# Kernel tuning notes

Measured on AMD Instinct MI355X. Metric: run time of the kernel, lower is better.

Reference implementation:

```python
import jax, jax.numpy as jnp
import numpy as np

HEADS = 8

def setup_inputs() -> dict:
    key = jax.random.key(0)
    k1, k2, k3 = jax.random.split(key, 3)
    B, C, L = 8, 512, 4096
    dim_head = 64
    hidden = HEADS * dim_head  # 512
    x = jax.random.normal(k1, (B, C, L), dtype=jnp.float32)
    # Conv1d(dim, hidden*3, 1, bias=False) -> weight [hidden*3, dim]
    w_qkv = jax.random.normal(k2, (hidden * 3, C), dtype=jnp.float32) * 0.02
    # Conv1d(hidden, dim, 1) -> weight [dim, hidden], bias [dim]
    w_out = jax.random.normal(k3, (C, hidden), dtype=jnp.float32) * 0.02
    b_out = jnp.zeros((C,), dtype=jnp.float32)
    return {"x": x, "w_qkv": w_qkv, "w_out": w_out, "b_out": b_out}

def reference(x, w_qkv, w_out, b_out):
    B, C, L = x.shape
    # 1x1 Conv1d == channel matmul
    qkv = jnp.einsum('oc,bcl->bol', w_qkv, x)            # [B, 3*H*dh, L]
    qkv = qkv.reshape(B, 3, HEADS, -1, L)                # qkv outermost, then heads, then c
    q, k, v = qkv[:, 0], qkv[:, 1], qkv[:, 2]            # each [B, H, dh, L]
    k = jax.nn.softmax(k, axis=-1)                       # softmax over sequence
    context = jnp.einsum('bhdn,bhen->bhde', k, v)        # [B, H, dh, dh]
    out = jnp.einsum('bhde,bhdn->bhen', context, q)      # [B, H, dh, L]
    out = out.reshape(B, -1, L)                          # [B, H*dh, L]
    return jnp.einsum('oc,bcl->bol', w_out, out) + b_out[None, :, None]
```

## Files before the change

### kernel.cpp

```cpp
#include <hip/hip_runtime.h>
#include <hip/hip_bf16.h>


typedef __bf16 bf16x8 __attribute__((ext_vector_type(8)));
typedef __bf16 bf16x4 __attribute__((ext_vector_type(4)));
typedef float  f32x4  __attribute__((ext_vector_type(4)));

#define B_  8
#define L_  4096
#define C_  512

#define GLD_LDS16(g, l)                                             \
    __builtin_amdgcn_global_load_lds(                               \
        (const __attribute__((address_space(1))) void*)(g),         \
        (__attribute__((address_space(3))) void*)(l), 16, 0, 0)

#define FENCE asm volatile("" ::: "memory")
#define BAR   do { FENCE; __builtin_amdgcn_s_barrier(); FENCE; } while (0)
#define DRAIN_LGKM asm volatile("s_waitcnt lgkmcnt(0)" ::: "memory")
#define WAIT_VM(N) asm volatile("s_waitcnt vmcnt(" #N ")" ::: "memory")

__global__ __launch_bounds__(256) void prep_all(const float* __restrict__ x,
                                                __hip_bfloat16* __restrict__ xt,
                                                const float* __restrict__ wqkv_f,
                                                __hip_bfloat16* __restrict__ wkv_b,
                                                __hip_bfloat16* __restrict__ wqT) {
    __shared__ float tile[64 * 132];
    int blk = blockIdx.x;
    int t = threadIdx.x;
    if (blk < 2048) {
        int b = blk >> 8, rem = blk & 255;
        int l0 = (rem & 31) * 128, c0 = (rem >> 5) * 64;
        const float* xp = x + ((size_t)b * C_ + c0) * L_ + l0;
#pragma unroll
        for (int p = 0; p < 8; p++) {
            int i = p * 8 + (t >> 5);
            int j = (t & 31) * 4;
            float4 vv = *(const float4*)(xp + (size_t)i * L_ + j);
            *(float4*)&tile[i * 132 + j] = vv;
        }
        __syncthreads();
        unsigned short* xo = (unsigned short*)xt + ((size_t)b * L_ + l0) * C_ + c0;
#pragma unroll
        for (int qq = 0; qq < 8; qq++) {
            int l = qq * 16 + (t >> 4);
            int cg = (t & 15) * 4;
            bf16x4 ov;
#pragma unroll
            for (int k = 0; k < 4; k++) ov[k] = (__bf16)tile[(cg + k) * 132 + l];
            *(bf16x4*)(xo + (size_t)l * C_ + cg) = ov;
        }
    } else if (blk < 4096) {
        int i = (blk - 2048) * 256 + t;
        wkv_b[i] = __float2bfloat16(wqkv_f[512 * 512 + i]);
    } else {
        int tb = blk - 4096;
        int r0 = (tb >> 4) * 32, c0 = (tb & 15) * 32;
        int tx = t & 31, ty = t >> 5;
        for (int r = 0; r < 32; r += 8)
            tile[(ty + r) * 33 + tx] = wqkv_f[(size_t)(r0 + ty + r) * 512 + c0 + tx];
        __syncthreads();
        for (int r = 0; r < 32; r += 8)
            wqT[(size_t)(c0 + ty + r) * 512 + r0 + tx] = __float2bfloat16(tile[tx * 33 + ty + r]);
    }
}

__global__ __launch_bounds__(256, 2) void gemm_kv(
    const __hip_bfloat16* __restrict__ A, const __hip_bfloat16* __restrict__ Bt,
    float* __restrict__ ctxp, float* __restrict__ Sp) {
    __shared__ alignas(16) unsigned short sA[2][128 * 64];
    __shared__ alignas(16) unsigned short sB[2][128 * 64];
    __shared__ float Sred[64];

    const int K = C_;
    int b = blockIdx.z, h = blockIdx.y, slice = blockIdx.x;
    const __hip_bfloat16* Bb = Bt + (size_t)b * L_ * C_;

    int t = threadIdx.x;
    int lane = t & 63, wv = t >> 6;
    int l16 = lane & 15, q4 = lane >> 4;
    int wr = (wv >> 1) * 64, wc = (wv & 1) * 64;

    int srow = lane >> 3;
    int swz  = ((lane & 7) ^ srow) * 8;

    if (t < 64) Sred[t] = 0.f;

    const __hip_bfloat16* gA[4];
    unsigned ldoff[4];
    int rloc[4];
#pragma unroll
    for (int c = 0; c < 4; c++) {
        int r = c * 32 + wv * 8;
        int lr = r + srow;
        int grow = h * 64 + lr + (lr >= 64 ? 448 : 0);
        gA[c] = A + (size_t)grow * K + swz;
        ldoff[c] = (unsigned)r * 64;
        rloc[c] = lr;
    }

    int gsel0 = (q4 ^ (l16 & 7)) * 8;
    int gsel1 = gsel0 ^ 32;
    unsigned rA = (unsigned)(wr + l16) * 64;
    unsigned rB = (unsigned)(wc + l16) * 64;
    const int NKT = K >> 6;

    f32x4 acc2[4] = {};
    bf16x8 aF[4][2], bF[4][2];

#pragma unroll 1
    for (int sub = 0; sub < 4; ++sub) {
        int nt = slice * 512 + sub * 128;
        const __hip_bfloat16* gB[4];
#pragma unroll
        for (int c = 0; c < 4; c++)
            gB[c] = Bb + (size_t)(nt + rloc[c]) * K + swz;

        f32x4 acc[4][4] = {};

#pragma unroll
        for (int c = 0; c < 4; c++) GLD_LDS16(gA[c], &sA[0][ldoff[c]]);
#pragma unroll
        for (int c = 0; c < 4; c++) GLD_LDS16(gB[c], &sB[0][ldoff[c]]);
#pragma unroll
        for (int c = 0; c < 4; c++) GLD_LDS16(gA[c] + 64, &sA[1][ldoff[c]]);
        WAIT_VM(4);
        BAR;

#pragma unroll 1
        for (int kt = 0; kt < NKT; ++kt) {
            int cur = kt & 1, nbuf = cur ^ 1;
            const unsigned short* As_b = sA[cur];
            const unsigned short* Bs_b = sB[cur];
            bool st1 = (kt + 1) < NKT;
            bool st2 = (kt + 2) < NKT;

#pragma unroll
            for (int i = 0; i < 4; i++) {
                aF[i][0] = *(const bf16x8*)&As_b[rA + i * 1024 + gsel0];
                aF[i][1] = *(const bf16x8*)&As_b[rA + i * 1024 + gsel1];
            }
#pragma unroll
            for (int j = 0; j < 2; j++) {
                bF[j][0] = *(const bf16x8*)&Bs_b[rB + j * 1024 + gsel0];
                bF[j][1] = *(const bf16x8*)&Bs_b[rB + j * 1024 + gsel1];
            }
            if (st1) {
                int ko = (kt + 1) << 6;
#pragma unroll
                for (int c = 0; c < 4; c++) GLD_LDS16(gB[c] + ko, &sB[nbuf][ldoff[c]]);
            }
            BAR;
            __builtin_amdgcn_s_setprio(1);
#pragma unroll
            for (int ks = 0; ks < 2; ks++)
#pragma unroll
                for (int i = 0; i < 4; i++)
#pragma unroll
                    for (int j = 0; j < 2; j++)
                        acc[i][j] = __builtin_amdgcn_mfma_f32_16x16x32_bf16(aF[i][ks], bF[j][ks], acc[i][j], 0, 0, 0);
            __builtin_amdgcn_s_setprio(0);
            DRAIN_LGKM;
            BAR;

#pragma unroll
            for (int j = 2; j < 4; j++) {
                bF[j][0] = *(const bf16x8*)&Bs_b[rB + j * 1024 + gsel0];
                bF[j][1] = *(const bf16x8*)&Bs_b[rB + j * 1024 + gsel1];
            }
            if (st2) {
                int ko = (kt + 2) << 6;
#pragma unroll
                for (int c = 0; c < 4; c++) GLD_LDS16(gA[c] + ko, &sA[cur][ldoff[c]]);
            }
            BAR;
            __builtin_amdgcn_s_setprio(1);
#pragma unroll
            for (int ks = 0; ks < 2; ks++)
#pragma unroll
                for (int i = 0; i < 4; i++)
#pragma unroll
                    for (int j = 0; j < 2; j++)
                        acc[i][2 + j] = __builtin_amdgcn_mfma_f32_16x16x32_bf16(aF[i][ks], bF[2 + j][ks], acc[i][2 + j], 0, 0, 0);
            __builtin_amdgcn_s_setprio(0);
            DRAIN_LGKM;
            if (st2) { WAIT_VM(4); } else { WAIT_VM(0); }
            BAR;
        }

        __bf16* Pb = (__bf16*)sA;
        __bf16* Vb = (__bf16*)sB;

        if (wv < 2) {
#pragma unroll
            for (int i = 0; i < 4; i++)
#pragma unroll
                for (int r = 0; r < 4; r++) {
                    int d = i * 16 + q4 * 4 + r;
                    float rs = 0.f;
#pragma unroll
                    for (int j = 0; j < 4; j++) {
                        int n = wc + j * 16 + l16;
                        float pv = __expf(acc[i][j][r]);
                        rs += pv;
                        Pb[d * 128 + (((n >> 3) ^ (d & 15)) * 8) + (n & 7)] = (__bf16)pv;
                    }
                    rs += __shfl_xor(rs, 1, 64);
                    rs += __shfl_xor(rs, 2, 64);
                    rs += __shfl_xor(rs, 4, 64);
                    rs += __shfl_xor(rs, 8, 64);
                    if (l16 == 0) atomicAdd(&Sred[d], rs);
                }
        } else {
#pragma unroll
            for (int i = 0; i < 4; i++)
#pragma unroll
                for (int j = 0; j < 4; j++)
#pragma unroll
                    for (int r = 0; r < 4; r++) {
                        int e = i * 16 + q4 * 4 + r;
                        int n = wc + j * 16 + l16;
                        Vb[e * 128 + (((n >> 3) ^ (e & 15)) * 8) + (n & 7)] = (__bf16)acc[i][j][r];
                    }
        }
        DRAIN_LGKM;
        BAR;

#pragma unroll
        for (int kk = 0; kk < 4; kk++) {
            int gg = kk * 4 + q4;
            bf16x8 bf2 = *(const bf16x8*)&Vb[(wv * 16 + l16) * 128 + ((gg ^ l16) * 8)];
#pragma unroll
            for (int i2 = 0; i2 < 4; i2++) {
                bf16x8 af2 = *(const bf16x8*)&Pb[(i2 * 16 + l16) * 128 + ((gg ^ l16) * 8)];
                acc2[i2] = __builtin_amdgcn_mfma_f32_16x16x32_bf16(af2, bf2, acc2[i2], 0, 0, 0);
            }
        }
        DRAIN_LGKM;
        BAR;
    }

    float* cg = ctxp + ((size_t)slice * 64 + b * 8 + h) * 4096;
#pragma unroll
    for (int i2 = 0; i2 < 4; i2++)
#pragma unroll
        for (int r = 0; r < 4; r++) {
            int d = i2 * 16 + q4 * 4 + r;
            int e = wv * 16 + l16;
            cg[d * 64 + e] = acc2[i2][r];
        }
    if (t < 64)
        Sp[((size_t)slice * 64 + b * 8 + h) * 64 + t] = Sred[t];
}

__global__ __launch_bounds__(256, 2) void gemm_p(
    const __hip_bfloat16* __restrict__ A, const __hip_bfloat16* __restrict__ Bt,
    size_t strideA, size_t strideB, int M, int N, int K,
    float* __restrict__ outb, const float* __restrict__ bias) {
    __shared__ alignas(16) unsigned short sA[2][128 * 64];
    __shared__ alignas(16) unsigned short sB[2][128 * 64];

    int b = blockIdx.z;
    int m0 = blockIdx.y * 128, n0 = blockIdx.x * 128;
    const __hip_bfloat16* Ab = A + strideA * (size_t)b;
    const __hip_bfloat16* Bb = Bt + strideB * (size_t)b;

    int t = threadIdx.x;
    int lane = t & 63, wv = t >> 6;
    int l16 = lane & 15, q4 = lane >> 4;
    int wr = (wv >> 1) * 64, wc = (wv & 1) * 64;

    int srow = lane >> 3;
    int swz  = ((lane & 7) ^ srow) * 8;

    const __hip_bfloat16* gA[4];
    const __hip_bfloat16* gB[4];
    unsigned ldoff[4];
#pragma unroll
    for (int c = 0; c < 4; c++) {
        int r = c * 32 + wv * 8;
        gA[c] = Ab + (size_t)(m0 + r + srow) * K + swz;
        gB[c] = Bb + (size_t)(n0 + r + srow) * K + swz;
        ldoff[c] = (unsigned)r * 64;
    }

    int gsel0 = (q4 ^ (l16 & 7)) * 8;
    int gsel1 = gsel0 ^ 32;
    unsigned rA = (unsigned)(wr + l16) * 64;
    unsigned rB = (unsigned)(wc + l16) * 64;
    int NKT = K >> 6;

    f32x4 acc[4][4] = {};
    bf16x8 aF[4][2], bF[4][2];

#pragma unroll
    for (int c = 0; c < 4; c++) GLD_LDS16(gA[c], &sA[0][ldoff[c]]);
#pragma unroll
    for (int c = 0; c < 4; c++) GLD_LDS16(gB[c], &sB[0][ldoff[c]]);
    if (NKT > 1) {
#pragma unroll
        for (int c = 0; c < 4; c++) GLD_LDS16(gA[c] + 64, &sA[1][ldoff[c]]);
        WAIT_VM(4);
    } else {
        WAIT_VM(0);
    }
    BAR;

#pragma unroll 1
    for (int kt = 0; kt < NKT; ++kt) {
        int cur = kt & 1, nbuf = cur ^ 1;
        const unsigned short* As_b = sA[cur];
        const unsigned short* Bs_b = sB[cur];
        bool st1 = (kt + 1) < NKT;
        bool st2 = (kt + 2) < NKT;

#pragma unroll
        for (int i = 0; i < 4; i++) {
            aF[i][0] = *(const bf16x8*)&As_b[rA + i * 1024 + gsel0];
            aF[i][1] = *(const bf16x8*)&As_b[rA + i * 1024 + gsel1];
        }
#pragma unroll
        for (int j = 0; j < 2; j++) {
            bF[j][0] = *(const bf16x8*)&Bs_b[rB + j * 1024 + gsel0];
            bF[j][1] = *(const bf16x8*)&Bs_b[rB + j * 1024 + gsel1];
        }
        if (st1) {
            int ko = (kt + 1) << 6;
#pragma unroll
            for (int c = 0; c < 4; c++) GLD_LDS16(gB[c] + ko, &sB[nbuf][ldoff[c]]);
        }
        BAR;
        __builtin_amdgcn_s_setprio(1);
#pragma unroll
        for (int ks = 0; ks < 2; ks++)
#pragma unroll
            for (int i = 0; i < 4; i++)
#pragma unroll
                for (int j = 0; j < 2; j++)
                    acc[i][j] = __builtin_amdgcn_mfma_f32_16x16x32_bf16(aF[i][ks], bF[j][ks], acc[i][j], 0, 0, 0);
        __builtin_amdgcn_s_setprio(0);
        DRAIN_LGKM;
        BAR;

#pragma unroll
        for (int j = 2; j < 4; j++) {
            bF[j][0] = *(const bf16x8*)&Bs_b[rB + j * 1024 + gsel0];
            bF[j][1] = *(const bf16x8*)&Bs_b[rB + j * 1024 + gsel1];
        }
        if (st2) {
            int ko = (kt + 2) << 6;
#pragma unroll
            for (int c = 0; c < 4; c++) GLD_LDS16(gA[c] + ko, &sA[cur][ldoff[c]]);
        }
        BAR;
        __builtin_amdgcn_s_setprio(1);
#pragma unroll
        for (int ks = 0; ks < 2; ks++)
#pragma unroll
            for (int i = 0; i < 4; i++)
#pragma unroll
                for (int j = 0; j < 2; j++)
                    acc[i][2 + j] = __builtin_amdgcn_mfma_f32_16x16x32_bf16(aF[i][ks], bF[2 + j][ks], acc[i][2 + j], 0, 0, 0);
        __builtin_amdgcn_s_setprio(0);
        DRAIN_LGKM;
        if (st2) { WAIT_VM(4); } else { WAIT_VM(0); }
        BAR;
    }

#pragma unroll
    for (int i = 0; i < 4; i++)
#pragma unroll
        for (int j = 0; j < 4; j++)
#pragma unroll
            for (int r = 0; r < 4; r++) {
                int row = m0 + wr + i * 16 + q4 * 4 + r;
                int col = n0 + wc + j * 16 + l16;
                outb[((size_t)b * M + row) * (size_t)N + col] = acc[i][j][r] + bias[row];
            }
}

__global__ __launch_bounds__(256) void gemm_bt(
    const __hip_bfloat16* __restrict__ A, const __hip_bfloat16* __restrict__ Bt,
    size_t strideA, size_t strideB, int M, int N, int K,
    __hip_bfloat16* __restrict__ obf) {
    __shared__ alignas(16) unsigned short As[128 * 64];
    __shared__ alignas(16) unsigned short Bs[128 * 64];

    int b = blockIdx.z;
    int m0 = blockIdx.y * 128, n0 = blockIdx.x * 128;
    const __hip_bfloat16* Ab = A + strideA * (size_t)b;
    const __hip_bfloat16* Bb = Bt + strideB * (size_t)b;

    int t = threadIdx.x;
    int lane = t & 63, wv = t >> 6;
    int l16 = lane & 15, q4 = lane >> 4;
    int wr = (wv >> 1) * 64, wc = (wv & 1) * 64;

    int srow = lane >> 3;
    int swz  = ((lane & 7) ^ srow) * 8;

    const __hip_bfloat16* gA[4];
    const __hip_bfloat16* gB[4];
    unsigned short* lA[4];
    unsigned short* lB[4];
#pragma unroll
    for (int c = 0; c < 4; c++) {
        int r = wv * 32 + c * 8;
        gA[c] = Ab + (size_t)(m0 + r + srow) * K + swz;
        gB[c] = Bb + (size_t)(n0 + r + srow) * K + swz;
        lA[c] = &As[r * 64];
        lB[c] = &Bs[r * 64];
    }

    int gsel0 = ((q4) ^ (l16 & 7)) * 8;
    int gsel1 = gsel0 ^ 32;
    int rA = (wr + l16) * 64;
    int rB = (wc + l16) * 64;

    f32x4 acc[4][4] = {};

    for (int k0 = 0; k0 < K; k0 += 64) {
        __syncthreads();
#pragma unroll
        for (int c = 0; c < 4; c++) {
            GLD_LDS16(gA[c] + k0, lA[c]);
            GLD_LDS16(gB[c] + k0, lB[c]);
        }
        __syncthreads();

        bf16x8 af[4], bfr[4];
#pragma unroll
        for (int i = 0; i < 4; i++) {
            af[i]  = *(const bf16x8*)&As[rA + i * 1024 + gsel0];
            bfr[i] = *(const bf16x8*)&Bs[rB + i * 1024 + gsel0];
        }
#pragma unroll
        for (int i = 0; i < 4; i++)
#pragma unroll
            for (int j = 0; j < 4; j++)
                acc[i][j] = __builtin_amdgcn_mfma_f32_16x16x32_bf16(af[i], bfr[j], acc[i][j], 0, 0, 0);
#pragma unroll
        for (int i = 0; i < 4; i++) {
            af[i]  = *(const bf16x8*)&As[rA + i * 1024 + gsel1];
            bfr[i] = *(const bf16x8*)&Bs[rB + i * 1024 + gsel1];
        }
#pragma unroll
        for (int i = 0; i < 4; i++)
#pragma unroll
            for (int j = 0; j < 4; j++)
                acc[i][j] = __builtin_amdgcn_mfma_f32_16x16x32_bf16(af[i], bfr[j], acc[i][j], 0, 0, 0);
    }

#pragma unroll
    for (int i = 0; i < 4; i++)
#pragma unroll
        for (int j = 0; j < 4; j++)
#pragma unroll
            for (int r = 0; r < 4; r++) {
                int row = m0 + wr + i * 16 + q4 * 4 + r;
                int col = n0 + wc + j * 16 + l16;
                obf[((size_t)b * 512 + row) * (size_t)N + col] = __float2bfloat16(acc[i][j][r]);
            }
}

__global__ __launch_bounds__(256) void w2_kernel(const float* __restrict__ wout,
                                                 const float* __restrict__ ctxp,
                                                 const float* __restrict__ Sp,
                                                 __hip_bfloat16* __restrict__ w2) {
    int ob = blockIdx.x, h = blockIdx.y, b = blockIdx.z;
    __shared__ float cT[64 * 65];
    __shared__ float wT[64 * 65];
    __shared__ float Sinv[64];
    int t = threadIdx.x;
    const size_t SL = (size_t)64 * 4096;
    const float* cg = ctxp + ((size_t)b * 8 + h) * 4096;
    if (t < 64) {
        const float* sg = Sp + ((size_t)b * 8 + h) * 64;
        float S = 0.f;
#pragma unroll
        for (int s = 0; s < 8; s++) S += sg[(size_t)s * 64 * 64 + t];
        Sinv[t] = 1.0f / S;
    }
    __syncthreads();
    for (int i = t; i < 4096; i += 256) {
        int d = i >> 6, e = i & 63;
        float s = 0.f;
#pragma unroll
        for (int sl = 0; sl < 8; sl++) s += cg[(size_t)sl * SL + i];
        cT[e * 65 + d] = s * Sinv[d];
        wT[e * 65 + d] = wout[(size_t)(ob * 64 + d) * 512 + h * 64 + e];
    }
    __syncthreads();
    int ol = t >> 2;
    int db = (t & 3) * 16;
    unsigned short* w2p = (unsigned short*)w2 + ((size_t)b * 512 + ob * 64 + ol) * 512 + h * 64;
    for (int g = 0; g < 4; g++) {
        int d0 = db + g * 4;
        float s0 = 0.f, s1 = 0.f, s2 = 0.f, s3 = 0.f;
#pragma unroll
        for (int e = 0; e < 64; e++) {
            float w = wT[e * 65 + ol];
            s0 += w * cT[e * 65 + d0];
            s1 += w * cT[e * 65 + d0 + 1];
            s2 += w * cT[e * 65 + d0 + 2];
            s3 += w * cT[e * 65 + d0 + 3];
        }
        bf16x4 ov;
        ov[0] = (__bf16)s0; ov[1] = (__bf16)s1; ov[2] = (__bf16)s2; ov[3] = (__bf16)s3;
        *(bf16x4*)(w2p + d0) = ov;
    }
}

extern "C" void kernel_launch(void* const* d_in, const int* in_sizes, int n_in,
                              void* d_out, int out_size, void* d_ws, size_t ws_size,
                              hipStream_t stream) {
    const float* x     = (const float*)d_in[0];
    const float* w_qkv = (const float*)d_in[1];
    const float* w_out = (const float*)d_in[2];
    const float* b_out = (const float*)d_in[3];
    float* out = (float*)d_out;
    char* ws = (char*)d_ws;

    size_t off_xt   = 0;
    size_t off_wkv  = off_xt + (size_t)B_ * L_ * C_ * 2;
    size_t off_wqT  = off_wkv + (size_t)1024 * 512 * 2;
    size_t off_ctxp = off_wqT + (size_t)512 * 512 * 2;
    size_t off_Sp   = off_ctxp + (size_t)8 * 64 * 4096 * 4;
    size_t off_w2   = off_Sp + (size_t)8 * 64 * 64 * 4;
    size_t off_w3   = off_w2 + (size_t)B_ * 512 * 512 * 2;

    __hip_bfloat16* xt   = (__hip_bfloat16*)(ws + off_xt);
    __hip_bfloat16* wkvb = (__hip_bfloat16*)(ws + off_wkv);
    __hip_bfloat16* wqT  = (__hip_bfloat16*)(ws + off_wqT);
    float*          ctxp = (float*)(ws + off_ctxp);
    float*          Sp   = (float*)(ws + off_Sp);
    __hip_bfloat16* w2   = (__hip_bfloat16*)(ws + off_w2);
    __hip_bfloat16* W3   = (__hip_bfloat16*)(ws + off_w3);

    prep_all<<<4352, 256, 0, stream>>>(x, xt, w_qkv, wkvb, wqT);

    gemm_kv<<<dim3(8, 8, B_), 256, 0, stream>>>(wkvb, xt, ctxp, Sp);

    w2_kernel<<<dim3(8, 8, B_), 256, 0, stream>>>(w_out, ctxp, Sp, w2);

    gemm_bt<<<dim3(512 / 128, 512 / 128, B_), 256, 0, stream>>>(
        w2, wqT, (size_t)512 * 512, 0, 512, 512, 512, W3);

    gemm_p<<<dim3(L_ / 128, 512 / 128, B_), 256, 0, stream>>>(
        W3, xt, (size_t)512 * 512, (size_t)L_ * C_, 512, L_, 512, out, b_out);
}
```

Baseline: 287.7 us.

## Split KV context GEMM across more blocks and add separate context reduction kernel

The kv GEMM is re-gridded from 8 slices, each looping over four 128-column sub-tiles, to 32 independent blocks per (batch, head), one 128-column tile each. This raises parallelism from 512 to 2048 blocks. A new ctxred kernel sums the 32 partial contexts, and w2_kernel now reads the reduced context with vectorised loads. The W2×Wq GEMM reuses the double-buffered gemm_p template in place of the simpler gemm_bt, and the x transpose writes 8-wide bf16 stores with a padded LDS stride. The cost is more partial-sum traffic and one extra launch.

```diff
diff --git a/kernel.cpp b/kernel.cpp
--- a/kernel.cpp
+++ b/kernel.cpp
@@ -25,7 +25,7 @@
                                                 const float* __restrict__ wqkv_f,
                                                 __hip_bfloat16* __restrict__ wkv_b,
                                                 __hip_bfloat16* __restrict__ wqT) {
-    __shared__ float tile[64 * 132];
+    __shared__ float tile[64 * 133];
     int blk = blockIdx.x;
     int t = threadIdx.x;
     if (blk < 2048) {
@@ -37,18 +37,18 @@
             int i = p * 8 + (t >> 5);
             int j = (t & 31) * 4;
             float4 vv = *(const float4*)(xp + (size_t)i * L_ + j);
-            *(float4*)&tile[i * 132 + j] = vv;
+            *(float4*)&tile[i * 133 + j] = vv;
         }
         __syncthreads();
         unsigned short* xo = (unsigned short*)xt + ((size_t)b * L_ + l0) * C_ + c0;
-#pragma unroll
-        for (int qq = 0; qq < 8; qq++) {
-            int l = qq * 16 + (t >> 4);
-            int cg = (t & 15) * 4;
-            bf16x4 ov;
-#pragma unroll
-            for (int k = 0; k < 4; k++) ov[k] = (__bf16)tile[(cg + k) * 132 + l];
-            *(bf16x4*)(xo + (size_t)l * C_ + cg) = ov;
+        int cg8 = (t & 7) * 8;
+#pragma unroll
+        for (int qq = 0; qq < 4; qq++) {
+            int l = qq * 32 + (t >> 3);
+            bf16x8 ov;
+#pragma unroll
+            for (int k = 0; k < 8; k++) ov[k] = (__bf16)tile[(cg8 + k) * 133 + l];
+            *(bf16x8*)(xo + (size_t)l * C_ + cg8) = ov;
         }
     } else if (blk < 4096) {
         int i = (blk - 2048) * 256 + t;
@@ -73,7 +73,8 @@
     __shared__ float Sred[64];
 
     const int K = C_;
-    int b = blockIdx.z, h = blockIdx.y, slice = blockIdx.x;
+    int b = blockIdx.z, h = blockIdx.y, nt = blockIdx.x;
+    int n0 = nt * 128;
     const __hip_bfloat16* Bb = Bt + (size_t)b * L_ * C_;
 
     int t = threadIdx.x;
@@ -87,16 +88,16 @@
     if (t < 64) Sred[t] = 0.f;
 
     const __hip_bfloat16* gA[4];
+    const __hip_bfloat16* gB[4];
     unsigned ldoff[4];
-    int rloc[4];
 #pragma unroll
     for (int c = 0; c < 4; c++) {
         int r = c * 32 + wv * 8;
         int lr = r + srow;
         int grow = h * 64 + lr + (lr >= 64 ? 448 : 0);
         gA[c] = A + (size_t)grow * K + swz;
+        gB[c] = Bb + (size_t)(n0 + lr) * K + swz;
         ldoff[c] = (unsigned)r * 64;
-        rloc[c] = lr;
     }
 
     int gsel0 = (q4 ^ (l16 & 7)) * 8;
@@ -105,191 +106,6 @@
     unsigned rB = (unsigned)(wc + l16) * 64;
     const int NKT = K >> 6;
 
-    f32x4 acc2[4] = {};
-    bf16x8 aF[4][2], bF[4][2];
-
-#pragma unroll 1
-    for (int sub = 0; sub < 4; ++sub) {
-        int nt = slice * 512 + sub * 128;
-        const __hip_bfloat16* gB[4];
-#pragma unroll
-        for (int c = 0; c < 4; c++)
-            gB[c] = Bb + (size_t)(nt + rloc[c]) * K + swz;
-
-        f32x4 acc[4][4] = {};
-
-#pragma unroll
-        for (int c = 0; c < 4; c++) GLD_LDS16(gA[c], &sA[0][ldoff[c]]);
-#pragma unroll
-        for (int c = 0; c < 4; c++) GLD_LDS16(gB[c], &sB[0][ldoff[c]]);
-#pragma unroll
-        for (int c = 0; c < 4; c++) GLD_LDS16(gA[c] + 64, &sA[1][ldoff[c]]);
-        WAIT_VM(4);
-        BAR;
-
-#pragma unroll 1
-        for (int kt = 0; kt < NKT; ++kt) {
-            int cur = kt & 1, nbuf = cur ^ 1;
-            const unsigned short* As_b = sA[cur];
-            const unsigned short* Bs_b = sB[cur];
-            bool st1 = (kt + 1) < NKT;
-            bool st2 = (kt + 2) < NKT;
-
-#pragma unroll
-            for (int i = 0; i < 4; i++) {
-                aF[i][0] = *(const bf16x8*)&As_b[rA + i * 1024 + gsel0];
-                aF[i][1] = *(const bf16x8*)&As_b[rA + i * 1024 + gsel1];
-            }
-#pragma unroll
-            for (int j = 0; j < 2; j++) {
-                bF[j][0] = *(const bf16x8*)&Bs_b[rB + j * 1024 + gsel0];
-                bF[j][1] = *(const bf16x8*)&Bs_b[rB + j * 1024 + gsel1];
-            }
-            if (st1) {
-                int ko = (kt + 1) << 6;
-#pragma unroll
-                for (int c = 0; c < 4; c++) GLD_LDS16(gB[c] + ko, &sB[nbuf][ldoff[c]]);
-            }
-            BAR;
-            __builtin_amdgcn_s_setprio(1);
-#pragma unroll
-            for (int ks = 0; ks < 2; ks++)
-#pragma unroll
-                for (int i = 0; i < 4; i++)
-#pragma unroll
-                    for (int j = 0; j < 2; j++)
-                        acc[i][j] = __builtin_amdgcn_mfma_f32_16x16x32_bf16(aF[i][ks], bF[j][ks], acc[i][j], 0, 0, 0);
-            __builtin_amdgcn_s_setprio(0);
-            DRAIN_LGKM;
-            BAR;
-
-#pragma unroll
-            for (int j = 2; j < 4; j++) {
-                bF[j][0] = *(const bf16x8*)&Bs_b[rB + j * 1024 + gsel0];
-                bF[j][1] = *(const bf16x8*)&Bs_b[rB + j * 1024 + gsel1];
-            }
-            if (st2) {
-                int ko = (kt + 2) << 6;
-#pragma unroll
-                for (int c = 0; c < 4; c++) GLD_LDS16(gA[c] + ko, &sA[cur][ldoff[c]]);
-            }
-            BAR;
-            __builtin_amdgcn_s_setprio(1);
-#pragma unroll
-            for (int ks = 0; ks < 2; ks++)
-#pragma unroll
-                for (int i = 0; i < 4; i++)
-#pragma unroll
-                    for (int j = 0; j < 2; j++)
-                        acc[i][2 + j] = __builtin_amdgcn_mfma_f32_16x16x32_bf16(aF[i][ks], bF[2 + j][ks], acc[i][2 + j], 0, 0, 0);
-            __builtin_amdgcn_s_setprio(0);
-            DRAIN_LGKM;
-            if (st2) { WAIT_VM(4); } else { WAIT_VM(0); }
-            BAR;
-        }
-
-        __bf16* Pb = (__bf16*)sA;
-        __bf16* Vb = (__bf16*)sB;
-
-        if (wv < 2) {
-#pragma unroll
-            for (int i = 0; i < 4; i++)
-#pragma unroll
-                for (int r = 0; r < 4; r++) {
-                    int d = i * 16 + q4 * 4 + r;
-                    float rs = 0.f;
-#pragma unroll
-                    for (int j = 0; j < 4; j++) {
-                        int n = wc + j * 16 + l16;
-                        float pv = __expf(acc[i][j][r]);
-                        rs += pv;
-                        Pb[d * 128 + (((n >> 3) ^ (d & 15)) * 8) + (n & 7)] = (__bf16)pv;
-                    }
-                    rs += __shfl_xor(rs, 1, 64);
-                    rs += __shfl_xor(rs, 2, 64);
-                    rs += __shfl_xor(rs, 4, 64);
-                    rs += __shfl_xor(rs, 8, 64);
-                    if (l16 == 0) atomicAdd(&Sred[d], rs);
-                }
-        } else {
-#pragma unroll
-            for (int i = 0; i < 4; i++)
-#pragma unroll
-                for (int j = 0; j < 4; j++)
-#pragma unroll
-                    for (int r = 0; r < 4; r++) {
-                        int e = i * 16 + q4 * 4 + r;
-                        int n = wc + j * 16 + l16;
-                        Vb[e * 128 + (((n >> 3) ^ (e & 15)) * 8) + (n & 7)] = (__bf16)acc[i][j][r];
-                    }
-        }
-        DRAIN_LGKM;
-        BAR;
-
-#pragma unroll
-        for (int kk = 0; kk < 4; kk++) {
-            int gg = kk * 4 + q4;
-            bf16x8 bf2 = *(const bf16x8*)&Vb[(wv * 16 + l16) * 128 + ((gg ^ l16) * 8)];
-#pragma unroll
-            for (int i2 = 0; i2 < 4; i2++) {
-                bf16x8 af2 = *(const bf16x8*)&Pb[(i2 * 16 + l16) * 128 + ((gg ^ l16) * 8)];
-                acc2[i2] = __builtin_amdgcn_mfma_f32_16x16x32_bf16(af2, bf2, acc2[i2], 0, 0, 0);
-            }
-        }
-        DRAIN_LGKM;
-        BAR;
-    }
-
-    float* cg = ctxp + ((size_t)slice * 64 + b * 8 + h) * 4096;
-#pragma unroll
-    for (int i2 = 0; i2 < 4; i2++)
-#pragma unroll
-        for (int r = 0; r < 4; r++) {
-            int d = i2 * 16 + q4 * 4 + r;
-            int e = wv * 16 + l16;
-            cg[d * 64 + e] = acc2[i2][r];
-        }
-    if (t < 64)
-        Sp[((size_t)slice * 64 + b * 8 + h) * 64 + t] = Sred[t];
-}
-
-__global__ __launch_bounds__(256, 2) void gemm_p(
-    const __hip_bfloat16* __restrict__ A, const __hip_bfloat16* __restrict__ Bt,
-    size_t strideA, size_t strideB, int M, int N, int K,
-    float* __restrict__ outb, const float* __restrict__ bias) {
-    __shared__ alignas(16) unsigned short sA[2][128 * 64];
-    __shared__ alignas(16) unsigned short sB[2][128 * 64];
-
-    int b = blockIdx.z;
-    int m0 = blockIdx.y * 128, n0 = blockIdx.x * 128;
-    const __hip_bfloat16* Ab = A + strideA * (size_t)b;
-    const __hip_bfloat16* Bb = Bt + strideB * (size_t)b;
-
-    int t = threadIdx.x;
-    int lane = t & 63, wv = t >> 6;
-    int l16 = lane & 15, q4 = lane >> 4;
-    int wr = (wv >> 1) * 64, wc = (wv & 1) * 64;
-
-    int srow = lane >> 3;
-    int swz  = ((lane & 7) ^ srow) * 8;
-
-    const __hip_bfloat16* gA[4];
-    const __hip_bfloat16* gB[4];
-    unsigned ldoff[4];
-#pragma unroll
-    for (int c = 0; c < 4; c++) {
-        int r = c * 32 + wv * 8;
-        gA[c] = Ab + (size_t)(m0 + r + srow) * K + swz;
-        gB[c] = Bb + (size_t)(n0 + r + srow) * K + swz;
-        ldoff[c] = (unsigned)r * 64;
-    }
-
-    int gsel0 = (q4 ^ (l16 & 7)) * 8;
-    int gsel1 = gsel0 ^ 32;
-    unsigned rA = (unsigned)(wr + l16) * 64;
-    unsigned rB = (unsigned)(wc + l16) * 64;
-    int NKT = K >> 6;
-
     f32x4 acc[4][4] = {};
     bf16x8 aF[4][2], bF[4][2];
 
@@ -297,13 +113,9 @@
     for (int c = 0; c < 4; c++) GLD_LDS16(gA[c], &sA[0][ldoff[c]]);
 #pragma unroll
     for (int c = 0; c < 4; c++) GLD_LDS16(gB[c], &sB[0][ldoff[c]]);
-    if (NKT > 1) {
-#pragma unroll
-        for (int c = 0; c < 4; c++) GLD_LDS16(gA[c] + 64, &sA[1][ldoff[c]]);
-        WAIT_VM(4);
-    } else {
-        WAIT_VM(0);
-    }
+#pragma unroll
+    for (int c = 0; c < 4; c++) GLD_LDS16(gA[c] + 64, &sA[1][ldoff[c]]);
+    WAIT_VM(4);
     BAR;
 
 #pragma unroll 1
@@ -367,24 +179,93 @@
         BAR;
     }
 
-#pragma unroll
-    for (int i = 0; i < 4; i++)
-#pragma unroll
-        for (int j = 0; j < 4; j++)
+    __bf16* Pb = (__bf16*)sA;
+    __bf16* Vb = (__bf16*)sB;
+
+    if (wv < 2) {
+#pragma unroll
+        for (int i = 0; i < 4; i++)
 #pragma unroll
             for (int r = 0; r < 4; r++) {
-                int row = m0 + wr + i * 16 + q4 * 4 + r;
-                int col = n0 + wc + j * 16 + l16;
-                outb[((size_t)b * M + row) * (size_t)N + col] = acc[i][j][r] + bias[row];
+                int d = i * 16 + q4 * 4 + r;
+                float rs = 0.f;
+#pragma unroll
+                for (int j = 0; j < 4; j++) {
+                    int n = wc + j * 16 + l16;
+                    float pv = __expf(acc[i][j][r]);
+                    rs += pv;
+                    Pb[d * 128 + (((n >> 3) ^ (d & 15)) * 8) + (n & 7)] = (__bf16)pv;
+                }
+                rs += __shfl_xor(rs, 1, 64);
+                rs += __shfl_xor(rs, 2, 64);
+                rs += __shfl_xor(rs, 4, 64);
+                rs += __shfl_xor(rs, 8, 64);
+                if (l16 == 0) atomicAdd(&Sred[d], rs);
             }
-}
-
-__global__ __launch_bounds__(256) void gemm_bt(
+    } else {
+#pragma unroll
+        for (int i = 0; i < 4; i++)
+#pragma unroll
+            for (int j = 0; j < 4; j++)
+#pragma unroll
+                for (int r = 0; r < 4; r++) {
+                    int e = i * 16 + q4 * 4 + r;
+                    int n = wc + j * 16 + l16;
+                    Vb[e * 128 + (((n >> 3) ^ (e & 15)) * 8) + (n & 7)] = (__bf16)acc[i][j][r];
+                }
+    }
+    DRAIN_LGKM;
+    BAR;
+
+    f32x4 acc2[4] = {};
+#pragma unroll
+    for (int kk = 0; kk < 4; kk++) {
+        int gg = kk * 4 + q4;
+        bf16x8 bf2 = *(const bf16x8*)&Vb[(wv * 16 + l16) * 128 + ((gg ^ l16) * 8)];
+#pragma unroll
+        for (int i2 = 0; i2 < 4; i2++) {
+            bf16x8 af2 = *(const bf16x8*)&Pb[(i2 * 16 + l16) * 128 + ((gg ^ l16) * 8)];
+            acc2[i2] = __builtin_amdgcn_mfma_f32_16x16x32_bf16(af2, bf2, acc2[i2], 0, 0, 0);
+        }
+    }
+
+    float* cg = ctxp + ((size_t)nt * 64 + b * 8 + h) * 4096;
+#pragma unroll
+    for (int i2 = 0; i2 < 4; i2++)
+#pragma unroll
+        for (int r = 0; r < 4; r++) {
+            int d = i2 * 16 + q4 * 4 + r;
+            int e = wv * 16 + l16;
+            cg[d * 64 + e] = acc2[i2][r];
+        }
+    if (t < 64)
+        Sp[((size_t)nt * 64 + b * 8 + h) * 64 + t] = Sred[t];
+}
+
+__global__ __launch_bounds__(256) void ctxred(const float* __restrict__ ctxp,
+                                              float* __restrict__ ctxs) {
+    int q = blockIdx.x;
+    int bh = blockIdx.y;
+    int t = threadIdx.x;
+    int i0 = q * 1024 + t * 4;
+    const float* cg = ctxp + (size_t)bh * 4096 + i0;
+    float4 s = {0.f, 0.f, 0.f, 0.f};
+#pragma unroll
+    for (int sl = 0; sl < 32; sl++) {
+        float4 v = *(const float4*)(cg + (size_t)sl * 64 * 4096);
+        s.x += v.x; s.y += v.y; s.z += v.z; s.w += v.w;
+    }
+    *(float4*)(ctxs + (size_t)bh * 4096 + i0) = s;
+}
+
+template <int MODE>
+__global__ __launch_bounds__(256, 2) void gemm_p(
     const __hip_bfloat16* __restrict__ A, const __hip_bfloat16* __restrict__ Bt,
     size_t strideA, size_t strideB, int M, int N, int K,
-    __hip_bfloat16* __restrict__ obf) {
-    __shared__ alignas(16) unsigned short As[128 * 64];
-    __shared__ alignas(16) unsigned short Bs[128 * 64];
+    __hip_bfloat16* __restrict__ obf,
+    float* __restrict__ outb, const float* __restrict__ bias) {
+    __shared__ alignas(16) unsigned short sA[2][128 * 64];
+    __shared__ alignas(16) unsigned short sB[2][128 * 64];
 
     int b = blockIdx.z;
     int m0 = blockIdx.y * 128, n0 = blockIdx.x * 128;
@@ -401,54 +282,96 @@
 
     const __hip_bfloat16* gA[4];
     const __hip_bfloat16* gB[4];
-    unsigned short* lA[4];
-    unsigned short* lB[4];
+    unsigned ldoff[4];
 #pragma unroll
     for (int c = 0; c < 4; c++) {
-        int r = wv * 32 + c * 8;
+        int r = c * 32 + wv * 8;
         gA[c] = Ab + (size_t)(m0 + r + srow) * K + swz;
         gB[c] = Bb + (size_t)(n0 + r + srow) * K + swz;
-        lA[c] = &As[r * 64];
-        lB[c] = &Bs[r * 64];
-    }
-
-    int gsel0 = ((q4) ^ (l16 & 7)) * 8;
+        ldoff[c] = (unsigned)r * 64;
+    }
+
+    int gsel0 = (q4 ^ (l16 & 7)) * 8;
     int gsel1 = gsel0 ^ 32;
-    int rA = (wr + l16) * 64;
-    int rB = (wc + l16) * 64;
+    unsigned rA = (unsigned)(wr + l16) * 64;
+    unsigned rB = (unsigned)(wc + l16) * 64;
+    int NKT = K >> 6;
 
     f32x4 acc[4][4] = {};
-
-    for (int k0 = 0; k0 < K; k0 += 64) {
-        __syncthreads();
-#pragma unroll
-        for (int c = 0; c < 4; c++) {
-            GLD_LDS16(gA[c] + k0, lA[c]);
-            GLD_LDS16(gB[c] + k0, lB[c]);
-        }
-        __syncthreads();
-
-        bf16x8 af[4], bfr[4];
+    bf16x8 aF[4][2], bF[4][2];
+
+#pragma unroll
+    for (int c = 0; c < 4; c++) GLD_LDS16(gA[c], &sA[0][ldoff[c]]);
+#pragma unroll
+    for (int c = 0; c < 4; c++) GLD_LDS16(gB[c], &sB[0][ldoff[c]]);
+    if (NKT > 1) {
+#pragma unroll
+        for (int c = 0; c < 4; c++) GLD_LDS16(gA[c] + 64, &sA[1][ldoff[c]]);
+        WAIT_VM(4);
+    } else {
+        WAIT_VM(0);
+    }
+    BAR;
+
+#pragma unroll 1
+    for (int kt = 0; kt < NKT; ++kt) {
+        int cur = kt & 1, nbuf = cur ^ 1;
+        const unsigned short* As_b = sA[cur];
+        const unsigned short* Bs_b = sB[cur];
+        bool st1 = (kt + 1) < NKT;
+        bool st2 = (kt + 2) < NKT;
+
 #pragma unroll
         for (int i = 0; i < 4; i++) {
-            af[i]  = *(const bf16x8*)&As[rA + i * 1024 + gsel0];
-            bfr[i] = *(const bf16x8*)&Bs[rB + i * 1024 + gsel0];
-        }
-#pragma unroll
-        for (int i = 0; i < 4; i++)
-#pragma unroll
-            for (int j = 0; j < 4; j++)
-                acc[i][j] = __builtin_amdgcn_mfma_f32_16x16x32_bf16(af[i], bfr[j], acc[i][j], 0, 0, 0);
-#pragma unroll
-        for (int i = 0; i < 4; i++) {
-            af[i]  = *(const bf16x8*)&As[rA + i * 1024 + gsel1];
-            bfr[i] = *(const bf16x8*)&Bs[rB + i * 1024 + gsel1];
-        }
-#pragma unroll
-        for (int i = 0; i < 4; i++)
-#pragma unroll
-            for (int j = 0; j < 4; j++)
-                acc[i][j] = __builtin_amdgcn_mfma_f32_16x16x32_bf16(af[i], bfr[j], acc[i][j], 0, 0, 0);
+            aF[i][0] = *(const bf16x8*)&As_b[rA + i * 1024 + gsel0];
+            aF[i][1] = *(const bf16x8*)&As_b[rA + i * 1024 + gsel1];
+        }
+#pragma unroll
+        for (int j = 0; j < 2; j++) {
+            bF[j][0] = *(const bf16x8*)&Bs_b[rB + j * 1024 + gsel0];
+            bF[j][1] = *(const bf16x8*)&Bs_b[rB + j * 1024 + gsel1];
+        }
+        if (st1) {
+            int ko = (kt + 1) << 6;
+#pragma unroll
+            for (int c = 0; c < 4; c++) GLD_LDS16(gB[c] + ko, &sB[nbuf][ldoff[c]]);
+        }
+        BAR;
+        __builtin_amdgcn_s_setprio(1);
+#pragma unroll
+        for (int ks = 0; ks < 2; ks++)
+#pragma unroll
+            for (int i = 0; i < 4; i++)
+#pragma unroll
+                for (int j = 0; j < 2; j++)
+                    acc[i][j] = __builtin_amdgcn_mfma_f32_16x16x32_bf16(aF[i][ks], bF[j][ks], acc[i][j], 0, 0, 0);
+        __builtin_amdgcn_s_setprio(0);
+        DRAIN_LGKM;
+        BAR;
+
+#pragma unroll
+        for (int j = 2; j < 4; j++) {
+            bF[j][0] = *(const bf16x8*)&Bs_b[rB + j * 1024 + gsel0];
+            bF[j][1] = *(const bf16x8*)&Bs_b[rB + j * 1024 + gsel1];
+        }
+        if (st2) {
+            int ko = (kt + 2) << 6;
+#pragma unroll
+            for (int c = 0; c < 4; c++) GLD_LDS16(gA[c] + ko, &sA[cur][ldoff[c]]);
+        }
+        BAR;
+        __builtin_amdgcn_s_setprio(1);
+#pragma unroll
+        for (int ks = 0; ks < 2; ks++)
+#pragma unroll
+            for (int i = 0; i < 4; i++)
+#pragma unroll
+                for (int j = 0; j < 2; j++)
+                    acc[i][2 + j] = __builtin_amdgcn_mfma_f32_16x16x32_bf16(aF[i][ks], bF[2 + j][ks], acc[i][2 + j], 0, 0, 0);
+        __builtin_amdgcn_s_setprio(0);
+        DRAIN_LGKM;
+        if (st2) { WAIT_VM(4); } else { WAIT_VM(0); }
+        BAR;
     }
 
 #pragma unroll
@@ -459,12 +382,17 @@
             for (int r = 0; r < 4; r++) {
                 int row = m0 + wr + i * 16 + q4 * 4 + r;
                 int col = n0 + wc + j * 16 + l16;
-                obf[((size_t)b * 512 + row) * (size_t)N + col] = __float2bfloat16(acc[i][j][r]);
+                float val = acc[i][j][r];
+                if (MODE == 3) {
+                    obf[((size_t)b * 512 + row) * (size_t)N + col] = __float2bfloat16(val);
+                } else {
+                    outb[((size_t)b * M + row) * (size_t)N + col] = val + bias[row];
+                }
             }
 }
 
 __global__ __launch_bounds__(256) void w2_kernel(const float* __restrict__ wout,
-                                                 const float* __restrict__ ctxp,
+                                                 const float* __restrict__ ctxs,
                                                  const float* __restrict__ Sp,
                                                  __hip_bfloat16* __restrict__ w2) {
     int ob = blockIdx.x, h = blockIdx.y, b = blockIdx.z;
@@ -472,23 +400,30 @@
     __shared__ float wT[64 * 65];
     __shared__ float Sinv[64];
     int t = threadIdx.x;
-    const size_t SL = (size_t)64 * 4096;
-    const float* cg = ctxp + ((size_t)b * 8 + h) * 4096;
+    const float* cg = ctxs + ((size_t)b * 8 + h) * 4096;
     if (t < 64) {
         const float* sg = Sp + ((size_t)b * 8 + h) * 64;
         float S = 0.f;
 #pragma unroll
-        for (int s = 0; s < 8; s++) S += sg[(size_t)s * 64 * 64 + t];
+        for (int s = 0; s < 32; s++) S += sg[(size_t)s * 64 * 64 + t];
         Sinv[t] = 1.0f / S;
     }
     __syncthreads();
-    for (int i = t; i < 4096; i += 256) {
-        int d = i >> 6, e = i & 63;
-        float s = 0.f;
-#pragma unroll
-        for (int sl = 0; sl < 8; sl++) s += cg[(size_t)sl * SL + i];
-        cT[e * 65 + d] = s * Sinv[d];
-        wT[e * 65 + d] = wout[(size_t)(ob * 64 + d) * 512 + h * 64 + e];
+#pragma unroll
+    for (int it = 0; it < 4; ++it) {
+        int i0 = (t + it * 256) * 4;
+        int d = i0 >> 6, e0 = i0 & 63;
+        float4 s4 = *(const float4*)&cg[i0];
+        float si = Sinv[d];
+        float4 wv4 = *(const float4*)&wout[(size_t)(ob * 64 + d) * 512 + h * 64 + e0];
+        cT[(e0 + 0) * 65 + d] = s4.x * si;
+        cT[(e0 + 1) * 65 + d] = s4.y * si;
+        cT[(e0 + 2) * 65 + d] = s4.z * si;
+        cT[(e0 + 3) * 65 + d] = s4.w * si;
+        wT[(e0 + 0) * 65 + d] = wv4.x;
+        wT[(e0 + 1) * 65 + d] = wv4.y;
+        wT[(e0 + 2) * 65 + d] = wv4.z;
+        wT[(e0 + 3) * 65 + d] = wv4.w;
     }
     __syncthreads();
     int ol = t >> 2;
@@ -525,8 +460,9 @@
     size_t off_wkv  = off_xt + (size_t)B_ * L_ * C_ * 2;
     size_t off_wqT  = off_wkv + (size_t)1024 * 512 * 2;
     size_t off_ctxp = off_wqT + (size_t)512 * 512 * 2;
-    size_t off_Sp   = off_ctxp + (size_t)8 * 64 * 4096 * 4;
-    size_t off_w2   = off_Sp + (size_t)8 * 64 * 64 * 4;
+    size_t off_Sp   = off_ctxp + (size_t)32 * 64 * 4096 * 4;
+    size_t off_ctxs = off_Sp + (size_t)32 * 64 * 64 * 4;
+    size_t off_w2   = off_ctxs + (size_t)64 * 4096 * 4;
     size_t off_w3   = off_w2 + (size_t)B_ * 512 * 512 * 2;
 
     __hip_bfloat16* xt   = (__hip_bfloat16*)(ws + off_xt);
@@ -534,18 +470,21 @@
     __hip_bfloat16* wqT  = (__hip_bfloat16*)(ws + off_wqT);
     float*          ctxp = (float*)(ws + off_ctxp);
     float*          Sp   = (float*)(ws + off_Sp);
+    float*          ctxs = (float*)(ws + off_ctxs);
     __hip_bfloat16* w2   = (__hip_bfloat16*)(ws + off_w2);
     __hip_bfloat16* W3   = (__hip_bfloat16*)(ws + off_w3);
 
     prep_all<<<4352, 256, 0, stream>>>(x, xt, w_qkv, wkvb, wqT);
 
-    gemm_kv<<<dim3(8, 8, B_), 256, 0, stream>>>(wkvb, xt, ctxp, Sp);
-
-    w2_kernel<<<dim3(8, 8, B_), 256, 0, stream>>>(w_out, ctxp, Sp, w2);
-
-    gemm_bt<<<dim3(512 / 128, 512 / 128, B_), 256, 0, stream>>>(
-        w2, wqT, (size_t)512 * 512, 0, 512, 512, 512, W3);
-
-    gemm_p<<<dim3(L_ / 128, 512 / 128, B_), 256, 0, stream>>>(
-        W3, xt, (size_t)512 * 512, (size_t)L_ * C_, 512, L_, 512, out, b_out);
-}
+    gemm_kv<<<dim3(L_ / 128, 8, B_), 256, 0, stream>>>(wkvb, xt, ctxp, Sp);
+
+    ctxred<<<dim3(4, 64), 256, 0, stream>>>(ctxp, ctxs);
+
+    w2_kernel<<<dim3(8, 8, B_), 256, 0, stream>>>(w_out, ctxs, Sp, w2);
+
+    gemm_p<3><<<dim3(512 / 128, 512 / 128, B_), 256, 0, stream>>>(
+        w2, wqT, (size_t)512 * 512, 0, 512, 512, 512, W3, nullptr, nullptr);
+
+    gemm_p<2><<<dim3(L_ / 128, 512 / 128, B_), 256, 0, stream>>>(
+        W3, xt, (size_t)512 * 512, (size_t)L_ * C_, 512, L_, 512, nullptr, out, b_out);
+}
```

New measurement: 231.8 us. 19.4% less time.
